# Optimization experiments

Measured on AMD Instinct MI355X. Metric: run time of the kernel, lower is better.

The kernel has to match this reference:

```python
import jax, jax.numpy as jnp
import numpy as np

B, X, Y, Z, C = 2, 96, 96, 64, 32
K_BG = K_FG = 8
LOG_PROB_SCALE = 200.0


def _make_gmm(key, K, C):
    k1, k2, k3 = jax.random.split(key, 3)
    # mixture weights divided by 2, as in the torch module
    w = jax.nn.softmax(jax.random.normal(k1, (K,))) / 2.0
    mu = jax.random.normal(k2, (K, C), dtype=jnp.float32)
    A = 0.1 * jax.random.normal(k3, (K, C, C), dtype=jnp.float32)
    d = 0.5 + jnp.abs(jnp.diagonal(A, axis1=-2, axis2=-1))  # positive diagonal
    L = jnp.tril(A, -1) + jax.vmap(jnp.diag)(d)             # valid lower Cholesky
    return w.astype(jnp.float32), mu, L


def setup_inputs() -> dict:
    key = jax.random.key(0)
    kf, kb, kg = jax.random.split(key, 3)
    feature_map = jax.random.normal(kf, (B, X, Y, Z, C), dtype=jnp.float32)
    w_bg, mu_bg, L_bg = _make_gmm(kb, K_BG, C)
    w_fg, mu_fg, L_fg = _make_gmm(kg, K_FG, C)
    return {
        "feature_map": feature_map,
        "weights_bg": w_bg, "means_bg": mu_bg, "chol_bg": L_bg,
        "weights_fg": w_fg, "means_fg": mu_fg, "chol_fg": L_fg,
    }


def reference(feature_map, weights_bg, means_bg, chol_bg,
              weights_fg, means_fg, chol_fg):
    Bv, Xv, Yv, Zv, Cv = feature_map.shape
    w = jnp.concatenate([weights_bg, weights_fg])      # [K]
    mu = jnp.concatenate([means_bg, means_fg])         # [K,C]
    L = jnp.concatenate([chol_bg, chol_fg])            # [K,C,C] lower tri

    eye = jnp.eye(Cv, dtype=L.dtype)
    Linv = jax.vmap(lambda l: jax.scipy.linalg.solve_triangular(l, eye, lower=True))(L)
    logdet = jnp.sum(jnp.log(jnp.diagonal(L, axis1=-2, axis2=-1)), axis=-1)  # [K]
    const = -0.5 * Cv * float(np.log(2.0 * np.pi))

    def body(dens, p):
        wk, muk, Lik, ldk = p
        # whitened residual y = L^{-1}(x - mu): [B,X,Y,Z,C]
        y = jnp.einsum('bxyzc,dc->bxyzd', feature_map - muk, Lik)
        logp = const - ldk - 0.5 * jnp.sum(y * y, axis=-1)  # MVN log_prob [B,X,Y,Z]
        return dens + wk * jnp.exp(logp / LOG_PROB_SCALE), None

    dens0 = jnp.zeros(feature_map.shape[:4], dtype=feature_map.dtype)
    dens, _ = jax.lax.scan(body, dens0, (w, mu, Linv, logdet))

    # torch loop runs frac in range(Z-1): last z-slice stays zero
    mask = (jnp.arange(Zv) < Zv - 1).astype(dens.dtype)
    dens = dens * mask  # broadcast over last axis
    return dens[:, None]  # [B,1,X,Y,Z]
```

## Files before the change

kernel.cpp:

```cpp
#include <hip/hip_runtime.h>
#include <hip/hip_bf16.h>
#include <cstring>

#define NVOX (2 * 96 * 96 * 64)
#define K_TOT 16
#define N_TILES (NVOX / 128)

typedef __attribute__((ext_vector_type(8)))  short short8;
typedef __attribute__((ext_vector_type(16))) float f32x16;
typedef __attribute__((ext_vector_type(2)))  float f32x2;

#define WS_UF 8192
#define WS_HW 8704
#define WS_FLOATS 8736

static __device__ __forceinline__ unsigned short f2b(float f) {
    __hip_bfloat16 h = __float2bfloat16(f);
    unsigned short u;
    __builtin_memcpy(&u, &h, 2);
    return u;
}

static __device__ __forceinline__ int pack2_bf16(float f0, float f1) {
    unsigned a, b;
    __builtin_memcpy(&a, &f0, 4);
    __builtin_memcpy(&b, &f1, 4);
    return (int)__builtin_amdgcn_perm(b + 0x8000u, a + 0x8000u, 0x07060302u);
}

static __device__ __forceinline__ short8 cvt8(float4 lo, float4 hi) {
    int p0 = pack2_bf16(lo.x, lo.y);
    int p1 = pack2_bf16(lo.z, lo.w);
    int p2 = pack2_bf16(hi.x, hi.y);
    int p3 = pack2_bf16(hi.z, hi.w);
    int v[4] = {p0, p1, p2, p3};
    short8 r;
    __builtin_memcpy(&r, v, 16);
    return r;
}

__global__ void gmm_prep_kernel(const float* __restrict__ wb, const float* __restrict__ mb,
                                const float* __restrict__ Lb, const float* __restrict__ wf,
                                const float* __restrict__ mf, const float* __restrict__ Lf,
                                float* __restrict__ ws) {
    int k   = blockIdx.x;
    int tid = threadIdx.x;

    __shared__ float Lsh[1024];
    __shared__ float Lish[1024];
    __shared__ float ush[32];

    const float* L  = (k < 8) ? (Lb + k * 1024) : (Lf + (k - 8) * 1024);
    const float* mu = (k < 8) ? (mb + k * 32)   : (mf + (k - 8) * 32);

    for (int i = tid; i < 1024; i += 64) Lsh[i] = L[i];
    __syncthreads();

    if (tid < 32) {
        int j = tid;
        float col[32];
#pragma unroll
        for (int i = 0; i < 32; ++i) {
            float s = (i == j) ? 1.0f : 0.0f;
#pragma unroll
            for (int m = 0; m < i; ++m) s = fmaf(-Lsh[i * 32 + m], col[m], s);
            float val = s / Lsh[i * 32 + i];
            col[i] = (i >= j) ? val : 0.0f;
        }
#pragma unroll
        for (int i = 0; i < 32; ++i) Lish[i * 32 + j] = col[i];
    }
    __syncthreads();
    if (tid < 32) {
        int d = tid;
        float s = 0.0f;
        for (int c = 0; c <= d; ++c) s = fmaf(Lish[d * 32 + c], mu[c], s);
        ush[d] = s;
    }
    __syncthreads();

    unsigned short* wsA = (unsigned short*)ws;
    int m  = tid & 31;
    int kq = tid >> 5;
#pragma unroll
    for (int hf = 0; hf < 2; ++hf) {
        unsigned short* dst = wsA + (size_t)(((k * 2 + hf) * 64 + tid) * 8);
#pragma unroll
        for (int j = 0; j < 8; ++j)
            dst[j] = f2b(Lish[m * 32 + hf * 16 + kq * 8 + j]);
    }
    if (tid < 32) {
        int h = tid >> 4, r = tid & 15;
        ws[WS_UF + k * 32 + tid] = -ush[(r & 3) + 8 * (r >> 2) + 4 * h];
    }
    if (tid == 0) {
        float ld = 0.0f;
        for (int i = 0; i < 32; ++i) ld += logf(Lsh[i * 32 + i]);
        const float cconst = -0.5f * 32.0f * 1.8378770664093453f;
        const float log2e  = 1.4426950408889634f;
        ws[WS_HW + k * 2]     = (cconst - ld) * (1.0f / 200.0f) * log2e;
        ws[WS_HW + k * 2 + 1] = (k < 8) ? wb[k] : wf[k - 8];
    }
}

__global__ __launch_bounds__(256, 3) void gmm_density_kernel(
        const float* __restrict__ fm, const float* __restrict__ ws,
        float* __restrict__ out) {
    __shared__ __align__(16) float smem[WS_FLOATS];
    {
        const float4* src = (const float4*)ws;
        float4* dst = (float4*)smem;
        for (int i = threadIdx.x; i < WS_FLOATS / 4; i += 256) dst[i] = src[i];
    }
    __syncthreads();
    const unsigned short* sWf = (const unsigned short*)smem;
    const float* sUf = smem + WS_UF;
    const float* sHW = smem + WS_HW;

    const int lane = threadIdx.x & 63;
    const int c    = lane & 31;
    const int h    = lane >> 5;
    const int tile = (blockIdx.x * 256 + (int)threadIdx.x) >> 6;
    size_t vbase = (size_t)tile * 128;

    const float SCALE = -0.0036067376022224085f;

    short8 Blo[4], Bhi[4];
#pragma unroll
    for (int g = 0; g < 4; ++g) {
        const float* xb = fm + (vbase + g * 32 + c) * 32 + h * 8;
        float4 a0 = *(const float4*)(xb + 0);
        float4 a1 = *(const float4*)(xb + 4);
        float4 b0 = *(const float4*)(xb + 16);
        float4 b1 = *(const float4*)(xb + 20);
        Blo[g] = cvt8(a0, a1);
        Bhi[g] = cvt8(b0, b1);
    }

    float dens[4] = {0.f, 0.f, 0.f, 0.f};
    for (int kc = 0; kc < K_TOT; ++kc) {
        short8 Alo = *(const short8*)(sWf + ((size_t)(kc * 2 + 0) * 64 + lane) * 8);
        short8 Ahi = *(const short8*)(sWf + ((size_t)(kc * 2 + 1) * 64 + lane) * 8);
        f32x16 Cu = *(const f32x16*)(sUf + kc * 32 + h * 16);
        float h2 = sHW[kc * 2], wk = sHW[kc * 2 + 1];
#pragma unroll
        for (int g = 0; g < 4; ++g) {
            f32x16 d = __builtin_amdgcn_mfma_f32_32x32x16_bf16(Alo, Blo[g], Cu, 0, 0, 0);
            d = __builtin_amdgcn_mfma_f32_32x32x16_bf16(Ahi, Bhi[g], d, 0, 0, 0);
            const f32x2* dp = (const f32x2*)&d;
            f32x2 acc0 = dp[0] * dp[0];
            f32x2 acc1 = dp[1] * dp[1];
#pragma unroll
            for (int r = 1; r < 4; ++r) {
                acc0 += dp[2 * r + 0] * dp[2 * r + 0];
                acc1 += dp[2 * r + 1] * dp[2 * r + 1];
            }
            f32x2 accs = acc0 + acc1;
            float p = accs[0] + accs[1];
            p += __shfl_xor(p, 32);
            dens[g] = fmaf(wk, __builtin_amdgcn_exp2f(fmaf(p, SCALE, h2)), dens[g]);
        }
    }

#pragma unroll
    for (int gg = 0; gg < 2; ++gg) {
        int g = h * 2 + gg;
        float val = dens[g];
        if (c == 31 && (g & 1)) val = 0.f;
        out[vbase + g * 32 + c] = val;
    }
}

extern "C" void kernel_launch(void* const* d_in, const int* in_sizes, int n_in,
                              void* d_out, int out_size, void* d_ws, size_t ws_size,
                              hipStream_t stream) {
    const float* fm = (const float*)d_in[0];
    const float* wb = (const float*)d_in[1];
    const float* mb = (const float*)d_in[2];
    const float* Lb = (const float*)d_in[3];
    const float* wf = (const float*)d_in[4];
    const float* mf = (const float*)d_in[5];
    const float* Lf = (const float*)d_in[6];
    float* out = (float*)d_out;
    float* ws  = (float*)d_ws;

    gmm_prep_kernel<<<K_TOT, 64, 0, stream>>>(wb, mb, Lb, wf, mf, Lf, ws);
    gmm_density_kernel<<<N_TILES / 4, 256, 0, stream>>>(fm, ws, out);
}
```

Before: 238.3 us.

## Make density kernel persistent with software-pipelined prefetch of next tile

```diff
diff --git a/kernel.cpp b/kernel.cpp
--- a/kernel.cpp
+++ b/kernel.cpp
@@ -5,10 +5,13 @@
 #define NVOX (2 * 96 * 96 * 64)
 #define K_TOT 16
 #define N_TILES (NVOX / 128)
+#define N_WAVES 3072
+#define N_BLOCKS 768
 
 typedef __attribute__((ext_vector_type(8)))  short short8;
 typedef __attribute__((ext_vector_type(16))) float f32x16;
 typedef __attribute__((ext_vector_type(2)))  float f32x2;
+typedef __attribute__((ext_vector_type(2)))  unsigned int uint2v;
 
 #define WS_UF 8192
 #define WS_HW 8704
@@ -39,6 +42,30 @@
     return r;
 }
 
+static __device__ __forceinline__ float rfl(float x) {
+    int i;
+    __builtin_memcpy(&i, &x, 4);
+    i = __builtin_amdgcn_readfirstlane(i);
+    float r;
+    __builtin_memcpy(&r, &i, 4);
+    return r;
+}
+
+static __device__ __forceinline__ float cross_half_sum(float p) {
+#if __has_builtin(__builtin_amdgcn_permlane32_swap)
+    unsigned pu;
+    __builtin_memcpy(&pu, &p, 4);
+    uint2v r = __builtin_amdgcn_permlane32_swap(pu, pu, false, false);
+    unsigned a = r.x, b = r.y;
+    float fa, fb;
+    __builtin_memcpy(&fa, &a, 4);
+    __builtin_memcpy(&fb, &b, 4);
+    return fa + fb;
+#else
+    return p + __shfl_xor(p, 32);
+#endif
+}
+
 __global__ void gmm_prep_kernel(const float* __restrict__ wb, const float* __restrict__ mb,
                                 const float* __restrict__ Lb, const float* __restrict__ wf,
                                 const float* __restrict__ mf, const float* __restrict__ Lf,
@@ -120,29 +147,47 @@
     const int lane = threadIdx.x & 63;
     const int c    = lane & 31;
     const int h    = lane >> 5;
-    const int tile = (blockIdx.x * 256 + (int)threadIdx.x) >> 6;
-    size_t vbase = (size_t)tile * 128;
+    const int wid  = (blockIdx.x * 256 + (int)threadIdx.x) >> 6;
 
     const float SCALE = -0.0036067376022224085f;
 
+    float h2s[K_TOT], wks[K_TOT];
+#pragma unroll
+    for (int k2 = 0; k2 < K_TOT; ++k2) {
+        h2s[k2] = rfl(sHW[k2 * 2]);
+        wks[k2] = rfl(sHW[k2 * 2 + 1]);
+    }
+
+    float4 raw[16];
     short8 Blo[4], Bhi[4];
-#pragma unroll
-    for (int g = 0; g < 4; ++g) {
-        const float* xb = fm + (vbase + g * 32 + c) * 32 + h * 8;
-        float4 a0 = *(const float4*)(xb + 0);
-        float4 a1 = *(const float4*)(xb + 4);
-        float4 b0 = *(const float4*)(xb + 16);
-        float4 b1 = *(const float4*)(xb + 20);
-        Blo[g] = cvt8(a0, a1);
-        Bhi[g] = cvt8(b0, b1);
-    }
-
-    float dens[4] = {0.f, 0.f, 0.f, 0.f};
-    for (int kc = 0; kc < K_TOT; ++kc) {
-        short8 Alo = *(const short8*)(sWf + ((size_t)(kc * 2 + 0) * 64 + lane) * 8);
-        short8 Ahi = *(const short8*)(sWf + ((size_t)(kc * 2 + 1) * 64 + lane) * 8);
-        f32x16 Cu = *(const f32x16*)(sUf + kc * 32 + h * 16);
-        float h2 = sHW[kc * 2], wk = sHW[kc * 2 + 1];
+
+    auto load_raw = [&](int tile) {
+        size_t vb = (size_t)tile * 128;
+#pragma unroll
+        for (int g = 0; g < 4; ++g) {
+            const float* xb = fm + (vb + g * 32 + c) * 32 + h * 8;
+            raw[g * 4 + 0] = *(const float4*)(xb + 0);
+            raw[g * 4 + 1] = *(const float4*)(xb + 4);
+            raw[g * 4 + 2] = *(const float4*)(xb + 16);
+            raw[g * 4 + 3] = *(const float4*)(xb + 20);
+        }
+    };
+    auto cvt_all = [&]() {
+#pragma unroll
+        for (int g = 0; g < 4; ++g) {
+            Blo[g] = cvt8(raw[g * 4 + 0], raw[g * 4 + 1]);
+            Bhi[g] = cvt8(raw[g * 4 + 2], raw[g * 4 + 3]);
+        }
+    };
+
+    load_raw(wid);
+    cvt_all();
+
+    float dens[4];
+    auto kstep = [&](int kc) {
+        const short8 Alo = *(const short8*)(sWf + ((size_t)(kc * 2 + 0) * 64 + lane) * 8);
+        const short8 Ahi = *(const short8*)(sWf + ((size_t)(kc * 2 + 1) * 64 + lane) * 8);
+        const f32x16 Cu  = *(const f32x16*)(sUf + kc * 32 + h * 16);
 #pragma unroll
         for (int g = 0; g < 4; ++g) {
             f32x16 d = __builtin_amdgcn_mfma_f32_32x32x16_bf16(Alo, Blo[g], Cu, 0, 0, 0);
@@ -157,17 +202,34 @@
             }
             f32x2 accs = acc0 + acc1;
             float p = accs[0] + accs[1];
-            p += __shfl_xor(p, 32);
-            dens[g] = fmaf(wk, __builtin_amdgcn_exp2f(fmaf(p, SCALE, h2)), dens[g]);
-        }
-    }
-
-#pragma unroll
-    for (int gg = 0; gg < 2; ++gg) {
-        int g = h * 2 + gg;
-        float val = dens[g];
-        if (c == 31 && (g & 1)) val = 0.f;
-        out[vbase + g * 32 + c] = val;
+            float pt = cross_half_sum(p);
+            dens[g] = fmaf(wks[kc], __builtin_amdgcn_exp2f(fmaf(pt, SCALE, h2s[kc])), dens[g]);
+        }
+    };
+
+#pragma unroll 1
+    for (int it = 0; it < 3; ++it) {
+        const int tile = wid + it * N_WAVES;
+        dens[0] = dens[1] = dens[2] = dens[3] = 0.f;
+
+#pragma unroll
+        for (int kc = 0; kc < 8; ++kc) kstep(kc);
+
+        if (it < 2) load_raw(wid + (it + 1) * N_WAVES);
+
+#pragma unroll
+        for (int kc = 8; kc < 16; ++kc) kstep(kc);
+
+        size_t vbase = (size_t)tile * 128;
+#pragma unroll
+        for (int gg = 0; gg < 2; ++gg) {
+            int g = h * 2 + gg;
+            float val = dens[g];
+            if (c == 31 && (g & 1)) val = 0.f;
+            out[vbase + g * 32 + c] = val;
+        }
+
+        if (it < 2) cvt_all();
     }
 }
 
@@ -185,5 +247,5 @@
     float* ws  = (float*)d_ws;
 
     gmm_prep_kernel<<<K_TOT, 64, 0, stream>>>(wb, mb, Lb, wf, mf, Lf, ws);
-    gmm_density_kernel<<<N_TILES / 4, 256, 0, stream>>>(fm, ws, out);
-}
+    gmm_density_kernel<<<N_BLOCKS, 256, 0, stream>>>(fm, ws, out);
+}
```

Measured after the change: 475.3 us. 1.99x slower.
